# Kernel tuning notes

Measured on AMD Instinct MI355X. Metric: run time of the kernel, lower is better.

The kernel has to match this reference:

```python
import jax, jax.numpy as jnp
import numpy as np

N = 200000   # atoms
M = 12       # neighbors per atom
F = 64       # atom_fea_len
NBR = 41     # nbr_fea_len
ORIG = 92    # orig_atom_fea_len
B = 2000     # crystals
SH = 9       # dim of 0e+1o+2e spherical harmonics (lmax=2)
NCONV = 3
HFEA = 128


def _sph_harm_l2(v):
    # real spherical harmonics up to l=2 on normalized vectors ('integral' norm)
    r = jnp.sqrt(jnp.sum(v * v, axis=-1, keepdims=True))
    u = v / jnp.maximum(r, 1e-9)
    x, y, z = u[..., 0], u[..., 1], u[..., 2]
    c0 = 0.28209479177387814   # 1/(2*sqrt(pi))
    c1 = 0.4886025119029199    # sqrt(3/(4*pi))
    c2 = 1.0925484305920792
    return jnp.stack([
        jnp.full_like(x, c0),
        c1 * y, c1 * z, c1 * x,
        c2 * x * y, c2 * y * z,
        0.31539156525252005 * (3.0 * z * z - 1.0),
        c2 * x * z,
        0.5462742152960396 * (x * x - y * y),
    ], axis=-1)


def setup_inputs() -> dict:
    key = jax.random.key(0)
    ks = jax.random.split(key, 12)
    s = 0.05
    return {
        "atom_fea": jax.random.normal(ks[0], (N, ORIG), jnp.float32),
        "nbr_fea": jax.random.uniform(ks[1], (N, M, NBR), dtype=jnp.float32),
        "nbr_idx": jax.random.randint(ks[2], (N, M), 0, N),
        "crystal_atom_idx": jnp.arange(N).reshape(B, N // B),
        "pos": jax.random.normal(ks[3], (N, 3), jnp.float32),
        "W_emb": jax.random.normal(ks[4], (ORIG, F), jnp.float32) * s,
        "b_emb": jnp.zeros((F,), jnp.float32),
        "Wr1": jax.random.normal(ks[5], (NCONV, NBR, NBR), jnp.float32) * s,
        "br1": jnp.zeros((NCONV, NBR), jnp.float32),
        "Wr2": jax.random.normal(ks[6], (NCONV, NBR, SH), jnp.float32) * s,
        "br2": jnp.zeros((NCONV, SH), jnp.float32),
        "Wtp": jax.random.normal(ks[7], (NCONV, F, F), jnp.float32) * s,
        "W_fc": jax.random.normal(ks[8], (F, HFEA), jnp.float32) * s,
        "b_fc": jnp.zeros((HFEA,), jnp.float32),
        "W_out": jax.random.normal(ks[9], (HFEA, 1), jnp.float32) * s,
        "b_out": jnp.zeros((1,), jnp.float32),
    }


def reference(atom_fea, nbr_fea, nbr_idx, crystal_atom_idx, pos,
              W_emb, b_emb, Wr1, br1, Wr2, br2, Wtp, W_fc, b_fc, W_out, b_out):
    x = atom_fea @ W_emb + b_emb                       # [N, F]
    src = nbr_idx.reshape(-1)                          # [N*M]
    e = nbr_fea.reshape(N * M, NBR)
    # dst = arange(N) repeated M times -> pos[dst] is just pos repeated
    rel = pos[src] - jnp.repeat(pos, M, axis=0)        # [N*M, 3]
    Y = _sph_harm_l2(rel)                              # [N*M, 9]
    Y0 = Y[:, :1]                                      # only 0e path feeds the TP output
    alpha = 1.0 / jnp.sqrt(jnp.float32(F))             # e3nn path normalization
    for l in range(NCONV):
        R = jax.nn.softplus(e @ Wr1[l] + br1[l]) @ Wr2[l] + br2[l]   # [N*M, 9]
        W0 = R[:, :1] * Y0                                           # scalar gate per edge
        msg = (x[src] @ Wtp[l]) * W0 * alpha                          # [N*M, F]
        # scatter-mean over dst == mean over the fixed M neighbors
        x = msg.reshape(N, M, F).mean(axis=1)
    crys = x[crystal_atom_idx].mean(axis=1)            # [B, F]
    h = jax.nn.softplus(crys @ W_fc + b_fc)            # [B, HFEA]
    out = h @ W_out + b_out                            # [B, 1]
    return (out, h)
```

## Files before the change

### kernel.cpp

```cpp
#include <hip/hip_runtime.h>
#include <hip/hip_bf16.h>
#include <math.h>

#define N_ATOMS 200000
#define M_NBR 12
#define F_DIM 64
#define NBR_FEA 41
#define ORIG_F 92
#define B_CRYS 2000
#define APB 100
#define SH_DIM 9
#define NCONV 3
#define HFEA 128
#define EDGES (N_ATOMS * M_NBR)

typedef __attribute__((ext_vector_type(8))) short short8;
typedef __attribute__((ext_vector_type(4))) float floatx4;

struct f4u { float x, y, z, w; };

__device__ __forceinline__ float softplus_f(float x) {
    return fmaxf(x, 0.0f) + __logf(1.0f + __expf(-fabsf(x)));
}
__device__ __forceinline__ unsigned short f2bf(float f) {
    __hip_bfloat16 h = __float2bfloat16(f);
    return *reinterpret_cast<unsigned short*>(&h);
}
__device__ __forceinline__ float bf2f(unsigned int u) {
    unsigned int x = u << 16;
    union { unsigned int i; float f; } c; c.i = x; return c.f;
}

__global__ __launch_bounds__(256) void k_embed(
    const float* __restrict__ atom_fea, const float* __restrict__ W_emb,
    const float* __restrict__ b_emb, unsigned short* __restrict__ x)
{
    __shared__ float ldsW[ORIG_F * F_DIM];
    __shared__ float ldsA[16 * ORIG_F];
    int tid = threadIdx.x;
    for (int i = tid; i < ORIG_F * F_DIM; i += 256) ldsW[i] = W_emb[i];
    long base = (long)blockIdx.x * 16;
    for (int i = tid; i < 16 * ORIG_F; i += 256) ldsA[i] = atom_fea[base * ORIG_F + i];
    __syncthreads();
    int col = tid & 63;
    int rg  = tid >> 6;
    float a0 = 0.f, a1 = 0.f, a2 = 0.f, a3 = 0.f;
    const float* Ar = &ldsA[(rg * 4) * ORIG_F];
    for (int k = 0; k < ORIG_F; ++k) {
        float wv = ldsW[k * F_DIM + col];
        a0 = fmaf(Ar[0 * ORIG_F + k], wv, a0);
        a1 = fmaf(Ar[1 * ORIG_F + k], wv, a1);
        a2 = fmaf(Ar[2 * ORIG_F + k], wv, a2);
        a3 = fmaf(Ar[3 * ORIG_F + k], wv, a3);
    }
    float bb = b_emb[col];
    long o = (base + rg * 4) * F_DIM + col;
    x[o]             = f2bf(a0 + bb);
    x[o + F_DIM]     = f2bf(a1 + bb);
    x[o + 2 * F_DIM] = f2bf(a2 + bb);
    x[o + 3 * F_DIM] = f2bf(a3 + bb);
}

__global__ __launch_bounds__(256) void k_prep(
    const float* __restrict__ Wr1, const float* __restrict__ br1,
    const float* __restrict__ Wr2, unsigned short* __restrict__ wpak,
    float* __restrict__ w2p, float* __restrict__ b1p)
{
    int t = threadIdx.x;
    for (int i = t; i < 64 * 18 * 8; i += 256) {
        int lane = i / 144;
        int rem  = i - lane * 144;
        int fid  = rem >> 3;
        int j    = rem & 7;
        int l  = fid / 6;
        int rf = fid - l * 6;
        int nt = rf >> 1;
        int s  = rf & 1;
        int n = nt * 16 + (lane & 15);
        int k = s * 32 + (lane >> 4) * 8 + j;
        unsigned short v = 0;
        if (n < NBR_FEA && k < NBR_FEA)
            v = f2bf(Wr1[(l * NBR_FEA + k) * NBR_FEA + n]);
        wpak[i] = v;
    }
    for (int i = t; i < 3 * 48; i += 256) {
        int l = i / 48, n = i - l * 48;
        w2p[i] = (n < NBR_FEA) ? Wr2[(l * NBR_FEA + n) * SH_DIM] : 0.f;
        b1p[i] = (n < NBR_FEA) ? br1[l * NBR_FEA + n] : 0.f;
    }
}

__global__ __launch_bounds__(256) void k_filter(
    const float* __restrict__ nbr_fea,
    const unsigned short* __restrict__ wpak,
    const float* __restrict__ w2p, const float* __restrict__ b1p,
    const float* __restrict__ br2, float* __restrict__ W0)
{
    int tid  = threadIdx.x;
    int lane = tid & 63;
    int wv   = tid >> 6;
    int sub  = lane & 15;
    int quad = lane >> 4;
    long ebase = (long)blockIdx.x * 256;

    short8 afr[4][2];
    #pragma unroll
    for (int mt = 0; mt < 4; ++mt) {
        long r = ebase + wv * 64 + mt * 16 + sub;
        const float* rowp = nbr_fea + r * NBR_FEA;
        f4u a = *(const f4u*)(rowp + quad * 8);
        f4u b = *(const f4u*)(rowp + quad * 8 + 4);
        short8 f0;
        f0[0] = (short)f2bf(a.x); f0[1] = (short)f2bf(a.y);
        f0[2] = (short)f2bf(a.z); f0[3] = (short)f2bf(a.w);
        f0[4] = (short)f2bf(b.x); f0[5] = (short)f2bf(b.y);
        f0[6] = (short)f2bf(b.z); f0[7] = (short)f2bf(b.w);
        afr[mt][0] = f0;
        short8 f1 = {0, 0, 0, 0, 0, 0, 0, 0};
        if (quad == 0) {
            f4u c = *(const f4u*)(rowp + 32);
            f4u d = *(const f4u*)(rowp + 36);
            f1[0] = (short)f2bf(c.x); f1[1] = (short)f2bf(c.y);
            f1[2] = (short)f2bf(c.z); f1[3] = (short)f2bf(c.w);
            f1[4] = (short)f2bf(d.x); f1[5] = (short)f2bf(d.y);
            f1[6] = (short)f2bf(d.z); f1[7] = (short)f2bf(d.w);
        } else if (quad == 1) {
            f1[0] = (short)f2bf(rowp[40]);
        }
        afr[mt][1] = f1;
    }

    const unsigned short* bbase = wpak + lane * 144;

    #pragma unroll
    for (int l = 0; l < NCONV; ++l) {
        short8 bfr[3][2];
        #pragma unroll
        for (int nt = 0; nt < 3; ++nt)
            #pragma unroll
            for (int s = 0; s < 2; ++s)
                bfr[nt][s] = *(const short8*)(bbase + ((l * 3 + nt) * 2 + s) * 8);

        floatx4 acc[4][3];
        #pragma unroll
        for (int mt = 0; mt < 4; ++mt)
            #pragma unroll
            for (int nt = 0; nt < 3; ++nt)
                acc[mt][nt] = (floatx4){0.f, 0.f, 0.f, 0.f};

        #pragma unroll
        for (int s = 0; s < 2; ++s)
            #pragma unroll
            for (int mt = 0; mt < 4; ++mt)
                #pragma unroll
                for (int nt = 0; nt < 3; ++nt)
                    acc[mt][nt] = __builtin_amdgcn_mfma_f32_16x16x32_bf16(
                        afr[mt][s], bfr[nt][s], acc[mt][nt], 0, 0, 0);

        float w2v[3], b1v[3];
        #pragma unroll
        for (int nt = 0; nt < 3; ++nt) {
            w2v[nt] = w2p[l * 48 + nt * 16 + sub];
            b1v[nt] = b1p[l * 48 + nt * 16 + sub];
        }
        float r2b = br2[l * SH_DIM];
        #pragma unroll
        for (int mt = 0; mt < 4; ++mt) {
            float p[4];
            #pragma unroll
            for (int reg = 0; reg < 4; ++reg) {
                float t = 0.f;
                #pragma unroll
                for (int nt = 0; nt < 3; ++nt)
                    t += softplus_f(acc[mt][nt][reg] + b1v[nt]) * w2v[nt];
                t += __shfl_xor(t, 1);
                t += __shfl_xor(t, 2);
                t += __shfl_xor(t, 4);
                t += __shfl_xor(t, 8);
                p[reg] = t + r2b;
            }
            if (sub == 0) {
                long base = (long)l * EDGES + ebase + wv * 64 + mt * 16 + quad * 4;
                *(floatx4*)&W0[base] = (floatx4){p[0], p[1], p[2], p[3]};
            }
        }
    }
}

__global__ __launch_bounds__(256) void k_conv(
    const unsigned short* __restrict__ x_in, const int* __restrict__ nbr_idx,
    const float* __restrict__ W0, const float* __restrict__ Wtp,
    unsigned short* __restrict__ x_out)
{
    __shared__ float g[16][F_DIM];
    int tid  = threadIdx.x;
    int lane = tid & 63;
    int wv   = tid >> 6;
    int aw   = lane >> 4;
    int fq   = lane & 15;
    const float cscale = 0.28209479177387814f * 0.125f / 12.0f;

    long atom = (long)blockIdx.x * 16 + wv * 4 + aw;
    long eb = atom * M_NBR;
    float4 acc = {0.f, 0.f, 0.f, 0.f};
    #pragma unroll
    for (int j = 0; j < M_NBR; ++j) {
        int   idx = nbr_idx[eb + j];
        float wj  = W0[eb + j];
        uint2 v = *(const uint2*)(x_in + (size_t)idx * F_DIM + fq * 4);
        acc.x = fmaf(wj, bf2f(v.x & 0xffffu), acc.x);
        acc.y = fmaf(wj, bf2f(v.x >> 16),     acc.y);
        acc.z = fmaf(wj, bf2f(v.y & 0xffffu), acc.z);
        acc.w = fmaf(wj, bf2f(v.y >> 16),     acc.w);
    }
    float4 gv = {acc.x * cscale, acc.y * cscale, acc.z * cscale, acc.w * cscale};
    *(float4*)&g[wv * 4 + aw][fq * 4] = gv;
    __syncthreads();

    int f = lane;
    float o0 = 0.f, o1 = 0.f, o2 = 0.f, o3 = 0.f;
    int r0 = wv * 4;
    for (int k4 = 0; k4 < F_DIM; k4 += 4) {
        float4 ga = *(const float4*)&g[r0 + 0][k4];
        float4 gb = *(const float4*)&g[r0 + 1][k4];
        float4 gc = *(const float4*)&g[r0 + 2][k4];
        float4 gd = *(const float4*)&g[r0 + 3][k4];
        #pragma unroll
        for (int t = 0; t < 4; ++t) {
            float wtv = Wtp[(k4 + t) * F_DIM + f];
            float gaa = (t == 0) ? ga.x : (t == 1) ? ga.y : (t == 2) ? ga.z : ga.w;
            float gbb = (t == 0) ? gb.x : (t == 1) ? gb.y : (t == 2) ? gb.z : gb.w;
            float gcc = (t == 0) ? gc.x : (t == 1) ? gc.y : (t == 2) ? gc.z : gc.w;
            float gdd = (t == 0) ? gd.x : (t == 1) ? gd.y : (t == 2) ? gd.z : gd.w;
            o0 = fmaf(gaa, wtv, o0);
            o1 = fmaf(gbb, wtv, o1);
            o2 = fmaf(gcc, wtv, o2);
            o3 = fmaf(gdd, wtv, o3);
        }
    }
    size_t ob = ((size_t)blockIdx.x * 16 + r0) * F_DIM + f;
    x_out[ob]             = f2bf(o0);
    x_out[ob + F_DIM]     = f2bf(o1);
    x_out[ob + 2 * F_DIM] = f2bf(o2);
    x_out[ob + 3 * F_DIM] = f2bf(o3);
}

__global__ __launch_bounds__(128) void k_readout(
    const unsigned short* __restrict__ x, const int* __restrict__ cidx,
    const float* __restrict__ W_fc, const float* __restrict__ b_fc,
    const float* __restrict__ W_out, const float* __restrict__ b_out,
    float* __restrict__ out, float* __restrict__ hout)
{
    __shared__ float part[2][F_DIM];
    __shared__ float crys[F_DIM];
    __shared__ float hw[HFEA];
    int tid = threadIdx.x;
    int c = blockIdx.x;
    int f = tid & 63, half = tid >> 6;
    const int* ci = cidx + c * APB + half * (APB / 2);
    float p = 0.f;
    for (int a = 0; a < APB / 2; ++a)
        p += bf2f(x[(size_t)ci[a] * F_DIM + f]);
    part[half][f] = p;
    __syncthreads();
    if (tid < F_DIM) crys[tid] = (part[0][tid] + part[1][tid]) * (1.0f / APB);
    __syncthreads();
    float acc = b_fc[tid];
    for (int ff = 0; ff < F_DIM; ++ff)
        acc = fmaf(crys[ff], W_fc[ff * HFEA + tid], acc);
    float h = softplus_f(acc);
    hout[(size_t)c * HFEA + tid] = h;
    hw[tid] = h * W_out[tid];
    __syncthreads();
    if (tid == 0) {
        float s = b_out[0];
        #pragma unroll 16
        for (int j = 0; j < HFEA; ++j) s += hw[j];
        out[c] = s;
    }
}

extern "C" void kernel_launch(void* const* d_in, const int* in_sizes, int n_in,
                              void* d_out, int out_size, void* d_ws, size_t ws_size,
                              hipStream_t stream) {
    const float* atom_fea = (const float*)d_in[0];
    const float* nbr_fea  = (const float*)d_in[1];
    const int*   nbr_idx  = (const int*)d_in[2];
    const int*   cidx     = (const int*)d_in[3];
    const float* W_emb = (const float*)d_in[5];
    const float* b_emb = (const float*)d_in[6];
    const float* Wr1   = (const float*)d_in[7];
    const float* br1   = (const float*)d_in[8];
    const float* Wr2   = (const float*)d_in[9];
    const float* br2   = (const float*)d_in[10];
    const float* Wtp   = (const float*)d_in[11];
    const float* W_fc  = (const float*)d_in[12];
    const float* b_fc  = (const float*)d_in[13];
    const float* W_out = (const float*)d_in[14];
    const float* b_out = (const float*)d_in[15];

    float* out  = (float*)d_out;
    float* hout = out + B_CRYS;

    float* W0 = (float*)d_ws;
    unsigned short* xA = (unsigned short*)(W0 + 3 * (size_t)EDGES);
    unsigned short* xB = xA + (size_t)N_ATOMS * F_DIM;

    unsigned short* wpak = xB;
    float* w2p = (float*)(wpak + 64 * 18 * 8);
    float* b1p = w2p + 3 * 48;

    k_prep  <<<1, 256, 0, stream>>>(Wr1, br1, Wr2, wpak, w2p, b1p);
    k_embed <<<N_ATOMS / 16, 256, 0, stream>>>(atom_fea, W_emb, b_emb, xA);
    k_filter<<<EDGES / 256, 256, 0, stream>>>(nbr_fea, wpak, w2p, b1p, br2, W0);
    k_conv  <<<N_ATOMS / 16, 256, 0, stream>>>(xA, nbr_idx, W0,             Wtp,                     xB);
    k_conv  <<<N_ATOMS / 16, 256, 0, stream>>>(xB, nbr_idx, W0 + EDGES,     Wtp + F_DIM * F_DIM,     xA);
    k_conv  <<<N_ATOMS / 16, 256, 0, stream>>>(xA, nbr_idx, W0 + 2 * EDGES, Wtp + 2 * F_DIM * F_DIM, xB);
    k_readout<<<B_CRYS, 128, 0, stream>>>(xB, cidx, W_fc, b_fc, W_out, b_out, out, hout);
}
```

Before: 983.8 us.

## Use MFMA for conv weight matmul and restructure filter MFMA epilogue

Each conv kernel now gathers neighbor features with wider 16-byte loads and handles 32 atoms per block. It stores the aggregated features as bf16 in a swizzled LDS tile and multiplies by pre-packed bf16 Wtp fragments with MFMA, replacing the scalar FP32 FMA loop. The filter kernel swaps MFMA operands so each lane holds edges along columns and seeds the accumulator with the bias. It also computes softplus via log2 with a pre-scaled weight and reduces with two shuffles instead of four. This adds bf16 rounding of the aggregated features, and the packed Wtp is placed in a scratch region inside the output buffer that the readout later overwrites.

```diff
diff --git a/kernel.cpp b/kernel.cpp
--- a/kernel.cpp
+++ b/kernel.cpp
@@ -19,9 +19,6 @@
 
 struct f4u { float x, y, z, w; };
 
-__device__ __forceinline__ float softplus_f(float x) {
-    return fmaxf(x, 0.0f) + __logf(1.0f + __expf(-fabsf(x)));
-}
 __device__ __forceinline__ unsigned short f2bf(float f) {
     __hip_bfloat16 h = __float2bfloat16(f);
     return *reinterpret_cast<unsigned short*>(&h);
@@ -29,6 +26,9 @@
 __device__ __forceinline__ float bf2f(unsigned int u) {
     unsigned int x = u << 16;
     union { unsigned int i; float f; } c; c.i = x; return c.f;
+}
+__device__ __forceinline__ float softplus_f(float x) {
+    return fmaxf(x, 0.0f) + __logf(1.0f + __expf(-fabsf(x)));
 }
 
 __global__ __launch_bounds__(256) void k_embed(
@@ -63,8 +63,9 @@
 
 __global__ __launch_bounds__(256) void k_prep(
     const float* __restrict__ Wr1, const float* __restrict__ br1,
-    const float* __restrict__ Wr2, unsigned short* __restrict__ wpak,
-    float* __restrict__ w2p, float* __restrict__ b1p)
+    const float* __restrict__ Wr2, const float* __restrict__ Wtp,
+    unsigned short* __restrict__ wpak, float* __restrict__ w2pk,
+    float* __restrict__ b1pk, unsigned short* __restrict__ wtpak)
 {
     int t = threadIdx.x;
     for (int i = t; i < 64 * 18 * 8; i += 256) {
@@ -83,17 +84,39 @@
             v = f2bf(Wr1[(l * NBR_FEA + k) * NBR_FEA + n]);
         wpak[i] = v;
     }
-    for (int i = t; i < 3 * 48; i += 256) {
-        int l = i / 48, n = i - l * 48;
-        w2p[i] = (n < NBR_FEA) ? Wr2[(l * NBR_FEA + n) * SH_DIM] : 0.f;
-        b1p[i] = (n < NBR_FEA) ? br1[l * NBR_FEA + n] : 0.f;
+    for (int i = t; i < 3 * 64 * 3 * 4; i += 256) {
+        int reg = i & 3;
+        int q   = i >> 2;
+        int nt  = q % 3;
+        int q2  = q / 3;
+        int lane = q2 & 63;
+        int l    = q2 >> 6;
+        int n = nt * 16 + (lane >> 4) * 4 + reg;
+        float b = 0.f, w = 0.f;
+        if (n < NBR_FEA) {
+            b = br1[l * NBR_FEA + n];
+            w = Wr2[(l * NBR_FEA + n) * SH_DIM];
+        }
+        b1pk[i] = b;
+        w2pk[i] = w;
+    }
+    for (int i = t; i < 3 * 64 * 64; i += 256) {
+        int j = i & 7;
+        int q = i >> 3;
+        int s = q & 1;  q >>= 1;
+        int nt = q & 3; q >>= 2;
+        int lane = q & 63;
+        int l    = q >> 6;
+        int k = s * 32 + (lane >> 4) * 8 + j;
+        int n = nt * 16 + (lane & 15);
+        wtpak[i] = f2bf(Wtp[(l * F_DIM + k) * F_DIM + n]);
     }
 }
 
 __global__ __launch_bounds__(256) void k_filter(
     const float* __restrict__ nbr_fea,
     const unsigned short* __restrict__ wpak,
-    const float* __restrict__ w2p, const float* __restrict__ b1p,
+    const float* __restrict__ w2pk, const float* __restrict__ b1pk,
     const float* __restrict__ br2, float* __restrict__ W0)
 {
     int tid  = threadIdx.x;
@@ -103,7 +126,7 @@
     int quad = lane >> 4;
     long ebase = (long)blockIdx.x * 256;
 
-    short8 afr[4][2];
+    short8 efr[4][2];
     #pragma unroll
     for (int mt = 0; mt < 4; ++mt) {
         long r = ebase + wv * 64 + mt * 16 + sub;
@@ -115,7 +138,7 @@
         f0[2] = (short)f2bf(a.z); f0[3] = (short)f2bf(a.w);
         f0[4] = (short)f2bf(b.x); f0[5] = (short)f2bf(b.y);
         f0[6] = (short)f2bf(b.z); f0[7] = (short)f2bf(b.w);
-        afr[mt][0] = f0;
+        efr[mt][0] = f0;
         short8 f1 = {0, 0, 0, 0, 0, 0, 0, 0};
         if (quad == 0) {
             f4u c = *(const f4u*)(rowp + 32);
@@ -127,122 +150,130 @@
         } else if (quad == 1) {
             f1[0] = (short)f2bf(rowp[40]);
         }
-        afr[mt][1] = f1;
-    }
-
-    const unsigned short* bbase = wpak + lane * 144;
+        efr[mt][1] = f1;
+    }
+
+    const unsigned short* abase = wpak + lane * 144;
 
     #pragma unroll
     for (int l = 0; l < NCONV; ++l) {
-        short8 bfr[3][2];
+        short8 wfr[3][2];
         #pragma unroll
         for (int nt = 0; nt < 3; ++nt)
             #pragma unroll
             for (int s = 0; s < 2; ++s)
-                bfr[nt][s] = *(const short8*)(bbase + ((l * 3 + nt) * 2 + s) * 8);
-
-        floatx4 acc[4][3];
-        #pragma unroll
-        for (int mt = 0; mt < 4; ++mt)
+                wfr[nt][s] = *(const short8*)(abase + ((l * 3 + nt) * 2 + s) * 8);
+
+        floatx4 b1v[3], w2v[3], w2l[3];
+        #pragma unroll
+        for (int nt = 0; nt < 3; ++nt) {
+            b1v[nt] = *(const floatx4*)&b1pk[((l * 64 + lane) * 3 + nt) * 4];
+            w2v[nt] = *(const floatx4*)&w2pk[((l * 64 + lane) * 3 + nt) * 4];
+            w2l[nt] = w2v[nt] * 0.69314718055994531f;
+        }
+
+        floatx4 acc[3][4];
+        #pragma unroll
+        for (int nt = 0; nt < 3; ++nt)
+            #pragma unroll
+            for (int mt = 0; mt < 4; ++mt)
+                acc[nt][mt] = b1v[nt];
+
+        #pragma unroll
+        for (int s = 0; s < 2; ++s)
             #pragma unroll
             for (int nt = 0; nt < 3; ++nt)
-                acc[mt][nt] = (floatx4){0.f, 0.f, 0.f, 0.f};
-
-        #pragma unroll
-        for (int s = 0; s < 2; ++s)
+                #pragma unroll
+                for (int mt = 0; mt < 4; ++mt)
+                    acc[nt][mt] = __builtin_amdgcn_mfma_f32_16x16x32_bf16(
+                        wfr[nt][s], efr[mt][s], acc[nt][mt], 0, 0, 0);
+
+        float r2b = br2[l * SH_DIM];
+        #pragma unroll
+        for (int mt = 0; mt < 4; ++mt) {
+            float t = 0.f;
             #pragma unroll
-            for (int mt = 0; mt < 4; ++mt)
+            for (int nt = 0; nt < 3; ++nt)
                 #pragma unroll
-                for (int nt = 0; nt < 3; ++nt)
-                    acc[mt][nt] = __builtin_amdgcn_mfma_f32_16x16x32_bf16(
-                        afr[mt][s], bfr[nt][s], acc[mt][nt], 0, 0, 0);
-
-        float w2v[3], b1v[3];
-        #pragma unroll
-        for (int nt = 0; nt < 3; ++nt) {
-            w2v[nt] = w2p[l * 48 + nt * 16 + sub];
-            b1v[nt] = b1p[l * 48 + nt * 16 + sub];
-        }
-        float r2b = br2[l * SH_DIM];
-        #pragma unroll
-        for (int mt = 0; mt < 4; ++mt) {
-            float p[4];
-            #pragma unroll
-            for (int reg = 0; reg < 4; ++reg) {
-                float t = 0.f;
-                #pragma unroll
-                for (int nt = 0; nt < 3; ++nt)
-                    t += softplus_f(acc[mt][nt][reg] + b1v[nt]) * w2v[nt];
-                t += __shfl_xor(t, 1);
-                t += __shfl_xor(t, 2);
-                t += __shfl_xor(t, 4);
-                t += __shfl_xor(t, 8);
-                p[reg] = t + r2b;
-            }
-            if (sub == 0) {
-                long base = (long)l * EDGES + ebase + wv * 64 + mt * 16 + quad * 4;
-                *(floatx4*)&W0[base] = (floatx4){p[0], p[1], p[2], p[3]};
-            }
+                for (int reg = 0; reg < 4; ++reg) {
+                    float x  = acc[nt][mt][reg];
+                    float e  = __expf(-fabsf(x));
+                    float lg = __log2f(1.0f + e);
+                    t = fmaf(fmaxf(x, 0.f), w2v[nt][reg], fmaf(lg, w2l[nt][reg], t));
+                }
+            t += __shfl_xor(t, 16);
+            t += __shfl_xor(t, 32);
+            if (quad == 0)
+                W0[(long)l * EDGES + ebase + wv * 64 + mt * 16 + sub] = t + r2b;
         }
     }
 }
 
 __global__ __launch_bounds__(256) void k_conv(
     const unsigned short* __restrict__ x_in, const int* __restrict__ nbr_idx,
-    const float* __restrict__ W0, const float* __restrict__ Wtp,
+    const float* __restrict__ W0, const unsigned short* __restrict__ wtp,
     unsigned short* __restrict__ x_out)
 {
-    __shared__ float g[16][F_DIM];
+    __shared__ __align__(16) unsigned short gl[32 * F_DIM];
     int tid  = threadIdx.x;
     int lane = tid & 63;
     int wv   = tid >> 6;
-    int aw   = lane >> 4;
-    int fq   = lane & 15;
+    int aw   = lane >> 3;
+    int oct  = lane & 7;
     const float cscale = 0.28209479177387814f * 0.125f / 12.0f;
 
-    long atom = (long)blockIdx.x * 16 + wv * 4 + aw;
-    long eb = atom * M_NBR;
-    float4 acc = {0.f, 0.f, 0.f, 0.f};
+    int  al   = wv * 8 + aw;
+    long atom = (long)blockIdx.x * 32 + al;
+    long eb   = atom * M_NBR;
+    float a0=0.f,a1=0.f,a2=0.f,a3=0.f,a4=0.f,a5=0.f,a6=0.f,a7=0.f;
     #pragma unroll
     for (int j = 0; j < M_NBR; ++j) {
         int   idx = nbr_idx[eb + j];
         float wj  = W0[eb + j];
-        uint2 v = *(const uint2*)(x_in + (size_t)idx * F_DIM + fq * 4);
-        acc.x = fmaf(wj, bf2f(v.x & 0xffffu), acc.x);
-        acc.y = fmaf(wj, bf2f(v.x >> 16),     acc.y);
-        acc.z = fmaf(wj, bf2f(v.y & 0xffffu), acc.z);
-        acc.w = fmaf(wj, bf2f(v.y >> 16),     acc.w);
-    }
-    float4 gv = {acc.x * cscale, acc.y * cscale, acc.z * cscale, acc.w * cscale};
-    *(float4*)&g[wv * 4 + aw][fq * 4] = gv;
-    __syncthreads();
-
-    int f = lane;
-    float o0 = 0.f, o1 = 0.f, o2 = 0.f, o3 = 0.f;
-    int r0 = wv * 4;
-    for (int k4 = 0; k4 < F_DIM; k4 += 4) {
-        float4 ga = *(const float4*)&g[r0 + 0][k4];
-        float4 gb = *(const float4*)&g[r0 + 1][k4];
-        float4 gc = *(const float4*)&g[r0 + 2][k4];
-        float4 gd = *(const float4*)&g[r0 + 3][k4];
-        #pragma unroll
-        for (int t = 0; t < 4; ++t) {
-            float wtv = Wtp[(k4 + t) * F_DIM + f];
-            float gaa = (t == 0) ? ga.x : (t == 1) ? ga.y : (t == 2) ? ga.z : ga.w;
-            float gbb = (t == 0) ? gb.x : (t == 1) ? gb.y : (t == 2) ? gb.z : gb.w;
-            float gcc = (t == 0) ? gc.x : (t == 1) ? gc.y : (t == 2) ? gc.z : gc.w;
-            float gdd = (t == 0) ? gd.x : (t == 1) ? gd.y : (t == 2) ? gd.z : gd.w;
-            o0 = fmaf(gaa, wtv, o0);
-            o1 = fmaf(gbb, wtv, o1);
-            o2 = fmaf(gcc, wtv, o2);
-            o3 = fmaf(gdd, wtv, o3);
-        }
-    }
-    size_t ob = ((size_t)blockIdx.x * 16 + r0) * F_DIM + f;
-    x_out[ob]             = f2bf(o0);
-    x_out[ob + F_DIM]     = f2bf(o1);
-    x_out[ob + 2 * F_DIM] = f2bf(o2);
-    x_out[ob + 3 * F_DIM] = f2bf(o3);
+        uint4 v = *(const uint4*)(x_in + (size_t)idx * F_DIM + oct * 8);
+        a0 = fmaf(wj, bf2f(v.x & 0xffffu), a0);
+        a1 = fmaf(wj, bf2f(v.x >> 16),     a1);
+        a2 = fmaf(wj, bf2f(v.y & 0xffffu), a2);
+        a3 = fmaf(wj, bf2f(v.y >> 16),     a3);
+        a4 = fmaf(wj, bf2f(v.z & 0xffffu), a4);
+        a5 = fmaf(wj, bf2f(v.z >> 16),     a5);
+        a6 = fmaf(wj, bf2f(v.w & 0xffffu), a6);
+        a7 = fmaf(wj, bf2f(v.w >> 16),     a7);
+    }
+    short8 pk;
+    pk[0] = (short)f2bf(a0 * cscale); pk[1] = (short)f2bf(a1 * cscale);
+    pk[2] = (short)f2bf(a2 * cscale); pk[3] = (short)f2bf(a3 * cscale);
+    pk[4] = (short)f2bf(a4 * cscale); pk[5] = (short)f2bf(a5 * cscale);
+    pk[6] = (short)f2bf(a6 * cscale); pk[7] = (short)f2bf(a7 * cscale);
+    int wb = (al * 128 + oct * 16) ^ ((al & 7) << 4);
+    *(short8*)((char*)gl + wb) = pk;
+    __syncthreads();
+
+    int sub = lane & 15, quad = lane >> 4;
+    int mt = wv & 1;
+    int nb = (wv >> 1) * 2;
+    short8 afr[2];
+    #pragma unroll
+    for (int s = 0; s < 2; ++s) {
+        int row = mt * 16 + sub;
+        int rb = (row * 128 + s * 64 + quad * 16) ^ ((row & 7) << 4);
+        afr[s] = *(const short8*)((const char*)gl + rb);
+    }
+    const unsigned short* bb = wtp + lane * 64;
+    floatx4 acc[2] = {{0.f,0.f,0.f,0.f},{0.f,0.f,0.f,0.f}};
+    #pragma unroll
+    for (int s = 0; s < 2; ++s)
+        #pragma unroll
+        for (int nti = 0; nti < 2; ++nti) {
+            short8 bfr = *(const short8*)(bb + (nb + nti) * 16 + s * 8);
+            acc[nti] = __builtin_amdgcn_mfma_f32_16x16x32_bf16(afr[s], bfr, acc[nti], 0, 0, 0);
+        }
+    size_t ob = ((size_t)blockIdx.x * 32 + mt * 16 + quad * 4) * F_DIM + nb * 16 + sub;
+    #pragma unroll
+    for (int nti = 0; nti < 2; ++nti)
+        #pragma unroll
+        for (int reg = 0; reg < 4; ++reg)
+            x_out[ob + (size_t)reg * F_DIM + nti * 16] = f2bf(acc[nti][reg]);
 }
 
 __global__ __launch_bounds__(128) void k_readout(
@@ -307,14 +338,15 @@
     unsigned short* xB = xA + (size_t)N_ATOMS * F_DIM;
 
     unsigned short* wpak = xB;
-    float* w2p = (float*)(wpak + 64 * 18 * 8);
-    float* b1p = w2p + 3 * 48;
-
-    k_prep  <<<1, 256, 0, stream>>>(Wr1, br1, Wr2, wpak, w2p, b1p);
+    float* w2pk = (float*)(wpak + 9216);
+    float* b1pk = w2pk + 2304;
+    unsigned short* wtpak = (unsigned short*)(hout + 128000);
+
+    k_prep  <<<1, 256, 0, stream>>>(Wr1, br1, Wr2, Wtp, wpak, w2pk, b1pk, wtpak);
     k_embed <<<N_ATOMS / 16, 256, 0, stream>>>(atom_fea, W_emb, b_emb, xA);
-    k_filter<<<EDGES / 256, 256, 0, stream>>>(nbr_fea, wpak, w2p, b1p, br2, W0);
-    k_conv  <<<N_ATOMS / 16, 256, 0, stream>>>(xA, nbr_idx, W0,             Wtp,                     xB);
-    k_conv  <<<N_ATOMS / 16, 256, 0, stream>>>(xB, nbr_idx, W0 + EDGES,     Wtp + F_DIM * F_DIM,     xA);
-    k_conv  <<<N_ATOMS / 16, 256, 0, stream>>>(xA, nbr_idx, W0 + 2 * EDGES, Wtp + 2 * F_DIM * F_DIM, xB);
+    k_filter<<<EDGES / 256, 256, 0, stream>>>(nbr_fea, wpak, w2pk, b1pk, br2, W0);
+    k_conv  <<<N_ATOMS / 32, 256, 0, stream>>>(xA, nbr_idx, W0,             wtpak,            xB);
+    k_conv  <<<N_ATOMS / 32, 256, 0, stream>>>(xB, nbr_idx, W0 + EDGES,     wtpak + 4096,     xA);
+    k_conv  <<<N_ATOMS / 32, 256, 0, stream>>>(xA, nbr_idx, W0 + 2 * EDGES, wtpak + 2 * 4096, xB);
     k_readout<<<B_CRYS, 128, 0, stream>>>(xB, cidx, W_fc, b_fc, W_out, b_out, out, hout);
 }
```

Result: faster. 923.6 us (-6.1%).
